# Kernel optimization log

Hardware: AMD Instinct MI355X
Metric: run time of the kernel (lower is better)

The kernel has to match this reference:

```python
import jax, jax.numpy as jnp
import numpy as np

K = 4

def grid_sample_bilinear_zeros(img, grid):
    # img: [b,c,H,W]; grid: [b,h,w,2] normalized coords (x,y) in [-1,1]
    # PyTorch grid_sample, mode='bilinear', padding_mode='zeros', align_corners=False
    b, c, H, W = img.shape
    h, w = grid.shape[1], grid.shape[2]
    ix = (grid[..., 0] + 1.0) * (W * 0.5) - 0.5
    iy = (grid[..., 1] + 1.0) * (H * 0.5) - 0.5
    x0 = jnp.floor(ix); y0 = jnp.floor(iy)
    wx1 = ix - x0; wx0 = 1.0 - wx1
    wy1 = iy - y0; wy0 = 1.0 - wy1
    x0i = x0.astype(jnp.int32); y0i = y0.astype(jnp.int32)
    x1i = x0i + 1; y1i = y0i + 1
    imgf = img.reshape(b, c, H * W)
    N = h * w

    def gather(xi, yi, wgt):
        valid = (xi >= 0) & (xi < W) & (yi >= 0) & (yi < H)
        xc = jnp.clip(xi, 0, W - 1); yc = jnp.clip(yi, 0, H - 1)
        idx = (yc * W + xc).reshape(b, 1, N)
        g = jnp.take_along_axis(imgf, jnp.broadcast_to(idx, (b, c, N)), axis=2)
        wv = (wgt * valid.astype(img.dtype)).reshape(b, 1, N)
        return g * wv

    out = (gather(x0i, y0i, wx0 * wy0) + gather(x1i, y0i, wx1 * wy0) +
           gather(x0i, y1i, wx0 * wy1) + gather(x1i, y1i, wx1 * wy1))
    return out.reshape(b, c, h, w)


def setup_inputs() -> dict:
    key = jax.random.key(0)
    ks = jax.random.split(key, 8)
    b, c, h, w = 8, 256, 96, 96
    out_ch = 256
    x = jax.random.normal(ks[0], (b, c, h, w), dtype=jnp.float32)
    Wc = jax.random.normal(ks[1], (out_ch, c), dtype=jnp.float32) * 0.02
    bc = jax.random.normal(ks[2], (out_ch,), dtype=jnp.float32) * 0.02
    Woff = jax.random.normal(ks[3], (K, 2, c), dtype=jnp.float32) * 0.02
    boff = jax.random.normal(ks[4], (K, 2), dtype=jnp.float32) * 0.02
    Wwt = jax.random.normal(ks[5], (K, c), dtype=jnp.float32) * 0.02
    bwt = jax.random.normal(ks[6], (K,), dtype=jnp.float32) * 0.02
    return {"x": x, "Wc": Wc, "bc": bc, "Woff": Woff, "boff": boff, "Wwt": Wwt, "bwt": bwt}


def reference(x, Wc, bc, Woff, boff, Wwt, bwt):
    b, c, h, w = x.shape
    # 1x1 conv projection
    proj = jnp.einsum('bchw,oc->bohw', x, Wc) + bc[None, :, None, None]
    # k flow fields, each [b,2,h,w] -> [k,b,h,w,2]
    flows = jnp.einsum('bchw,koc->kbohw', x, Woff) + boff[:, None, :, None, None]
    flows = jnp.transpose(flows, (0, 1, 3, 4, 2))
    # softmax sampling weights [b,k,h,w]
    logits = jnp.einsum('bchw,kc->bkhw', x, Wwt) + bwt[None, :, None, None]
    weights = jax.nn.softmax(logits, axis=1)
    # base pixel grid (x,y)
    gy, gx = jnp.meshgrid(jnp.arange(h, dtype=x.dtype), jnp.arange(w, dtype=x.dtype), indexing='ij')
    base = jnp.stack((gx, gy), axis=-1)  # [h,w,2]
    vgrid = base[None, None] + flows  # [k,b,h,w,2]
    vx = 2.0 * vgrid[..., 0] / max(w - 1, 1) - 1.0
    vy = 2.0 * vgrid[..., 1] / max(h - 1, 1) - 1.0
    vgrid_scaled = jnp.stack((vx, vy), axis=-1)  # [k,b,h,w,2]
    feats = jax.vmap(lambda g: grid_sample_bilinear_zeros(proj, g))(vgrid_scaled)  # [k,b,o,h,w]
    out = jnp.einsum('kbohw,bkhw->bohw', feats, weights)
    return out
```

## Files before the change

### kernel.cpp

```cpp
#include <hip/hip_runtime.h>

#define HW   9216
#define IMG  96
#define NB   8
#define NK   4

typedef __bf16 bf16x8 __attribute__((ext_vector_type(8)));
typedef float  f32x4  __attribute__((ext_vector_type(4)));

__device__ __forceinline__ unsigned short f2bf(float f) {
    unsigned int u = __float_as_uint(f);
    u += 0x7FFFu + ((u >> 16) & 1u);
    return (unsigned short)(u >> 16);
}

extern "C" __global__ __launch_bounds__(256, 4)
void prep_kernel(const float* __restrict__ x,
                 const float* __restrict__ Wc,
                 const float* __restrict__ Woff,
                 const float* __restrict__ boff,
                 const float* __restrict__ Wwt,
                 const float* __restrict__ bwt,
                 unsigned short* __restrict__ xbt,
                 unsigned short* __restrict__ Wcb,
                 float2* __restrict__ coords,
                 float* __restrict__ wts)
{
    __shared__ __align__(16) unsigned short tile[64 * 266];

    const int t   = threadIdx.x;
    const int bxr = blockIdx.x;

    if (bxr >= NB * 144) {
        int u = ((bxr - NB * 144) * 256 + t) * 4;
        float4 v = *(const float4*)(Wc + u);
        union { unsigned short h[4]; int2 p; } pk;
        pk.h[0] = f2bf(v.x); pk.h[1] = f2bf(v.y);
        pk.h[2] = f2bf(v.z); pk.h[3] = f2bf(v.w);
        *(int2*)(Wcb + u) = pk.p;
        return;
    }

    const int b  = bxr / 144;
    const int p0 = (bxr % 144) * 64;
    const int px = t & 63;
    const int g  = __builtin_amdgcn_readfirstlane(t >> 6);

    float acc[12];
    #pragma unroll
    for (int j = 0; j < 12; ++j) acc[j] = 0.f;

    const float* xb = x + ((size_t)(b * 256 + g * 64)) * HW + p0 + px;
    unsigned int* trow = (unsigned int*)tile;

    for (int i0 = 0; i0 < 64; i0 += 8) {
        float v[8];
        #pragma unroll
        for (int q = 0; q < 8; ++q)
            v[q] = xb[(size_t)(i0 + q) * HW];
        #pragma unroll
        for (int q = 0; q < 8; ++q) {
            const int c = g * 64 + i0 + q;
            #pragma unroll
            for (int j = 0; j < 8; ++j) acc[j] += v[q] * Woff[j * 256 + c];
            #pragma unroll
            for (int j = 0; j < 4; ++j) acc[8 + j] += v[q] * Wwt[j * 256 + c];
        }
        #pragma unroll
        for (int q = 0; q < 8; q += 2) {
            unsigned int pk = (unsigned int)f2bf(v[q]) | ((unsigned int)f2bf(v[q + 1]) << 16);
            trow[px * 133 + ((g * 64 + i0 + q) >> 1)] = pk;
        }
    }

    __syncthreads();
    #pragma unroll
    for (int r = 0; r < 8; ++r) {
        int u = t + 256 * r;
        int sub = u & 31, p2 = u >> 5;
        int4 v = *(const int4*)(tile + p2 * 266 + sub * 8);
        *(int4*)(xbt + ((size_t)b * HW + p0 + p2) * 256 + sub * 8) = v;
    }
    __syncthreads();

    float* red = (float*)tile;
    #pragma unroll
    for (int j = 0; j < 12; ++j)
        red[(g * 64 + px) * 12 + j] = acc[j];
    __syncthreads();

    if (t < 64) {
        float s[12];
        #pragma unroll
        for (int j = 0; j < 12; ++j)
            s[j] = red[(0 * 64 + px) * 12 + j] + red[(1 * 64 + px) * 12 + j] +
                   red[(2 * 64 + px) * 12 + j] + red[(3 * 64 + px) * 12 + j];

        const int p = p0 + px;
        const float pyf = (float)(p / IMG);
        const float pxf = (float)(p % IMG);

        #pragma unroll
        for (int k = 0; k < NK; ++k) {
            float fx = s[k * 2 + 0] + boff[k * 2 + 0];
            float fy = s[k * 2 + 1] + boff[k * 2 + 1];
            float vx = 2.0f * (pxf + fx) / 95.0f - 1.0f;
            float vy = 2.0f * (pyf + fy) / 95.0f - 1.0f;
            float ix = (vx + 1.0f) * 48.0f - 0.5f;
            float iy = (vy + 1.0f) * 48.0f - 0.5f;
            coords[((size_t)k * NB + b) * HW + p] = make_float2(ix, iy);
        }
        float l0 = s[8] + bwt[0], l1 = s[9] + bwt[1];
        float l2 = s[10] + bwt[2], l3 = s[11] + bwt[3];
        float m = fmaxf(fmaxf(l0, l1), fmaxf(l2, l3));
        float e0 = __expf(l0 - m), e1 = __expf(l1 - m);
        float e2 = __expf(l2 - m), e3 = __expf(l3 - m);
        float inv = 1.0f / (e0 + e1 + e2 + e3);
        wts[((size_t)0 * NB + b) * HW + p] = e0 * inv;
        wts[((size_t)1 * NB + b) * HW + p] = e1 * inv;
        wts[((size_t)2 * NB + b) * HW + p] = e2 * inv;
        wts[((size_t)3 * NB + b) * HW + p] = e3 * inv;
    }
}

extern "C" __global__ __launch_bounds__(256, 3)
void fused_kernel(const unsigned short* __restrict__ Wcb,
                  const unsigned short* __restrict__ xbt,
                  const float2* __restrict__ coords,
                  const float* __restrict__ wts,
                  const float* __restrict__ bc,
                  float* __restrict__ out)
{
    __shared__ __align__(16) unsigned char lds[49408];
    unsigned short* BsU   = (unsigned short*)lds;
    unsigned short* AsU   = (unsigned short*)(lds + 32768);
    float*          cw    = (float*)(lds + 32768);
    unsigned int*   ci    = (unsigned int*)(lds + 36864);
    float*          wsumL = (float*)(lds + 49152);

    const int t  = threadIdx.x;
    const int bx = blockIdx.x;
    const int b  = bx & 7;
    const int p0 = (bx >> 3) * 64;

    {
        const int px = t & 63;
        const int k  = t >> 6;
        const int p  = p0 + px;
        float2 cc = coords[((size_t)k * NB + b) * HW + p];
        float wk  = wts[((size_t)k * NB + b) * HW + p];
        float x0f = floorf(cc.x), y0f = floorf(cc.y);
        float wx1 = cc.x - x0f, wx0 = 1.0f - wx1;
        float wy1 = cc.y - y0f, wy0 = 1.0f - wy1;
        int x0 = (int)x0f, y0 = (int)y0f;
        int x1 = x0 + 1,   y1 = y0 + 1;
        float vx0 = (x0 >= 0 && x0 < IMG) ? 1.f : 0.f;
        float vx1 = (x1 >= 0 && x1 < IMG) ? 1.f : 0.f;
        float vy0 = (y0 >= 0 && y0 < IMG) ? 1.f : 0.f;
        float vy1 = (y1 >= 0 && y1 < IMG) ? 1.f : 0.f;
        int cx0 = min(max(x0, 0), IMG - 1), cx1 = min(max(x1, 0), IMG - 1);
        int cy0 = min(max(y0, 0), IMG - 1), cy1 = min(max(y1, 0), IMG - 1);
        int i0 = cy0 * IMG + cx0, i1 = cy0 * IMG + cx1;
        int i2 = cy1 * IMG + cx0, i3 = cy1 * IMG + cx1;
        float w0 = wk * wx0 * wy0 * vx0 * vy0;
        float w1 = wk * wx1 * wy0 * vx1 * vy0;
        float w2 = wk * wx0 * wy1 * vx0 * vy1;
        float w3 = wk * wx1 * wy1 * vx1 * vy1;
        *(float4*)(cw + px * 16 + k * 4) = make_float4(w0, w1, w2, w3);
        uint2 ip;
        ip.x = (unsigned int)i0 | ((unsigned int)i1 << 16);
        ip.y = (unsigned int)i2 | ((unsigned int)i3 << 16);
        *(uint2*)(ci + px * 8 + k * 2) = ip;
    }
    __syncthreads();

    {
        if (t < 64) {
            float s = 0.f;
            #pragma unroll
            for (int j = 0; j < 16; ++j) s += cw[t * 16 + j];
            wsumL[t] = s;
        }
        const int pxl = t >> 5, ch = t & 31;
        const unsigned short* gbase = xbt + (size_t)b * HW * 256 + ch * 8;
        #pragma unroll 2
        for (int rep = 0; rep < 8; ++rep) {
            const int px = rep * 8 + pxl;
            float wl[16];
            #pragma unroll
            for (int q = 0; q < 4; ++q) {
                float4 wv = *(const float4*)(cw + px * 16 + q * 4);
                wl[q * 4 + 0] = wv.x; wl[q * 4 + 1] = wv.y;
                wl[q * 4 + 2] = wv.z; wl[q * 4 + 3] = wv.w;
            }
            unsigned int ip[8];
            #pragma unroll
            for (int q = 0; q < 2; ++q) {
                uint4 iv = *(const uint4*)(ci + px * 8 + q * 4);
                ip[q * 4 + 0] = iv.x; ip[q * 4 + 1] = iv.y;
                ip[q * 4 + 2] = iv.z; ip[q * 4 + 3] = iv.w;
            }
            int4 v[16];
            #pragma unroll
            for (int j = 0; j < 16; ++j) {
                unsigned int idx = (ip[j >> 1] >> ((j & 1) * 16)) & 0xFFFFu;
                v[j] = *(const int4*)(gbase + (size_t)idx * 256);
            }
            float acc[8];
            #pragma unroll
            for (int i = 0; i < 8; ++i) acc[i] = 0.f;
            #pragma unroll
            for (int j = 0; j < 16; ++j) {
                const unsigned int* u = (const unsigned int*)&v[j];
                float wj = wl[j];
                #pragma unroll
                for (int q = 0; q < 4; ++q) {
                    float lo = __uint_as_float(u[q] << 16);
                    float hi = __uint_as_float(u[q] & 0xFFFF0000u);
                    acc[2 * q + 0] += wj * lo;
                    acc[2 * q + 1] += wj * hi;
                }
            }
            union { unsigned short h[8]; int4 v4; } pk;
            #pragma unroll
            for (int i = 0; i < 8; ++i) pk.h[i] = f2bf(acc[i]);
            const int pos = ch ^ (px & 7);
            *(int4*)(BsU + px * 256 + pos * 8) = pk.v4;
        }
    }
    __syncthreads();

    const int lane = t & 63, wave = t >> 6;
    const int wm = wave * 64;
    const int l15 = lane & 15, quad = lane >> 4;

    unsigned short* AsW = AsU + wave * 2048;

    f32x4 acc[4][4];
    #pragma unroll
    for (int mt = 0; mt < 4; ++mt)
        #pragma unroll
        for (int nt = 0; nt < 4; ++nt)
            acc[mt][nt] = (f32x4){0.f, 0.f, 0.f, 0.f};

#define STAGE_A(K0)                                                            \
    do {                                                                       \
        _Pragma("unroll")                                                      \
        for (int i_ = 0; i_ < 4; ++i_) {                                       \
            int u_ = lane + 64 * i_;                                           \
            int row_ = u_ >> 2, sub_ = u_ & 3;                                 \
            int subg_ = sub_ ^ ((row_ >> 1) & 3);                              \
            __builtin_amdgcn_global_load_lds(                                  \
                (const __attribute__((address_space(1))) void*)(               \
                    Wcb + (size_t)(wm + row_) * 256 + (K0) + subg_ * 8),       \
                (__attribute__((address_space(3))) void*)(AsW + u_ * 8),       \
                16, 0, 0);                                                     \
        }                                                                      \
    } while (0)

    STAGE_A(0);
    for (int k0 = 0; k0 < 256; k0 += 32) {
        asm volatile("s_waitcnt vmcnt(0)" ::: "memory");
        bf16x8 af[4], bf[4];
        #pragma unroll
        for (int mt = 0; mt < 4; ++mt) {
            int row = mt * 16 + l15;
            int pos = quad ^ ((row >> 1) & 3);
            af[mt] = *(const bf16x8*)(const void*)(AsW + row * 32 + pos * 8);
        }
        if (k0 + 32 < 256) {
            asm volatile("s_waitcnt lgkmcnt(0)" ::: "memory");
            __builtin_amdgcn_sched_barrier(0);
            STAGE_A(k0 + 32);
        }
        #pragma unroll
        for (int nt = 0; nt < 4; ++nt) {
            int row = nt * 16 + l15;
            int pos = ((k0 >> 3) + quad) ^ (row & 7);
            bf[nt] = *(const bf16x8*)(const void*)(BsU + row * 256 + pos * 8);
        }
        #pragma unroll
        for (int mt = 0; mt < 4; ++mt)
            #pragma unroll
            for (int nt = 0; nt < 4; ++nt)
                acc[mt][nt] = __builtin_amdgcn_mfma_f32_16x16x32_bf16(af[mt], bf[nt], acc[mt][nt], 0, 0, 0);
    }
#undef STAGE_A

    float wv[4];
    #pragma unroll
    for (int nt = 0; nt < 4; ++nt)
        wv[nt] = wsumL[nt * 16 + l15];

    #pragma unroll
    for (int mt = 0; mt < 4; ++mt) {
        int ob = wm + mt * 16 + quad * 4;
        #pragma unroll
        for (int reg = 0; reg < 4; ++reg) {
            int o = ob + reg;
            float bias = bc[o];
            float* dst = out + ((size_t)b * 256 + o) * HW + p0 + l15;
            #pragma unroll
            for (int nt = 0; nt < 4; ++nt)
                dst[nt * 16] = acc[mt][nt][reg] + bias * wv[nt];
        }
    }
}

extern "C" void kernel_launch(void* const* d_in, const int* in_sizes, int n_in,
                              void* d_out, int out_size, void* d_ws, size_t ws_size,
                              hipStream_t stream)
{
    const float* x    = (const float*)d_in[0];
    const float* Wc   = (const float*)d_in[1];
    const float* bc   = (const float*)d_in[2];
    const float* Woff = (const float*)d_in[3];
    const float* boff = (const float*)d_in[4];
    const float* Wwt  = (const float*)d_in[5];
    const float* bwt  = (const float*)d_in[6];
    float* out = (float*)d_out;

    char* ws = (char*)d_ws;
    unsigned short* xbt  = (unsigned short*)(ws);
    float2* coords       = (float2*)(ws + 37748736);
    float*  wts          = (float*)(ws + 40108032);
    unsigned short* Wcb  = (unsigned short*)(ws + 41287680);

    prep_kernel<<<dim3(NB * 144 + 64), dim3(256), 0, stream>>>(
        x, Wc, Woff, boff, Wwt, bwt, xbt, Wcb, coords, wts);
    fused_kernel<<<dim3(NB * 144), dim3(256), 0, stream>>>(
        Wcb, xbt, coords, wts, bc, out);
}
```

Before: 190.2 us.

## Double-buffer gather loads in fused kernel and widen prep blocks to 512 threads

```diff
diff --git a/kernel.cpp b/kernel.cpp
--- a/kernel.cpp
+++ b/kernel.cpp
@@ -14,7 +14,7 @@
     return (unsigned short)(u >> 16);
 }
 
-extern "C" __global__ __launch_bounds__(256, 4)
+extern "C" __global__ __launch_bounds__(512, 8)
 void prep_kernel(const float* __restrict__ x,
                  const float* __restrict__ Wc,
                  const float* __restrict__ Woff,
@@ -32,7 +32,7 @@
     const int bxr = blockIdx.x;
 
     if (bxr >= NB * 144) {
-        int u = ((bxr - NB * 144) * 256 + t) * 4;
+        int u = ((bxr - NB * 144) * 512 + t) * 4;
         float4 v = *(const float4*)(Wc + u);
         union { unsigned short h[4]; int2 p; } pk;
         pk.h[0] = f2bf(v.x); pk.h[1] = f2bf(v.y);
@@ -50,17 +50,17 @@
     #pragma unroll
     for (int j = 0; j < 12; ++j) acc[j] = 0.f;
 
-    const float* xb = x + ((size_t)(b * 256 + g * 64)) * HW + p0 + px;
+    const float* xb = x + ((size_t)(b * 256 + g * 32)) * HW + p0 + px;
     unsigned int* trow = (unsigned int*)tile;
 
-    for (int i0 = 0; i0 < 64; i0 += 8) {
+    for (int i0 = 0; i0 < 32; i0 += 8) {
         float v[8];
         #pragma unroll
         for (int q = 0; q < 8; ++q)
             v[q] = xb[(size_t)(i0 + q) * HW];
         #pragma unroll
         for (int q = 0; q < 8; ++q) {
-            const int c = g * 64 + i0 + q;
+            const int c = g * 32 + i0 + q;
             #pragma unroll
             for (int j = 0; j < 8; ++j) acc[j] += v[q] * Woff[j * 256 + c];
             #pragma unroll
@@ -69,14 +69,14 @@
         #pragma unroll
         for (int q = 0; q < 8; q += 2) {
             unsigned int pk = (unsigned int)f2bf(v[q]) | ((unsigned int)f2bf(v[q + 1]) << 16);
-            trow[px * 133 + ((g * 64 + i0 + q) >> 1)] = pk;
-        }
-    }
-
-    __syncthreads();
-    #pragma unroll
-    for (int r = 0; r < 8; ++r) {
-        int u = t + 256 * r;
+            trow[px * 133 + ((g * 32 + i0 + q) >> 1)] = pk;
+        }
+    }
+
+    __syncthreads();
+    #pragma unroll
+    for (int r = 0; r < 4; ++r) {
+        int u = t + 512 * r;
         int sub = u & 31, p2 = u >> 5;
         int4 v = *(const int4*)(tile + p2 * 266 + sub * 8);
         *(int4*)(xbt + ((size_t)b * HW + p0 + p2) * 256 + sub * 8) = v;
@@ -92,9 +92,13 @@
     if (t < 64) {
         float s[12];
         #pragma unroll
-        for (int j = 0; j < 12; ++j)
-            s[j] = red[(0 * 64 + px) * 12 + j] + red[(1 * 64 + px) * 12 + j] +
-                   red[(2 * 64 + px) * 12 + j] + red[(3 * 64 + px) * 12 + j];
+        for (int j = 0; j < 12; ++j) {
+            float sj = 0.f;
+            #pragma unroll
+            for (int w = 0; w < 8; ++w)
+                sj += red[(w * 64 + px) * 12 + j];
+            s[j] = sj;
+        }
 
         const int p = p0 + px;
         const float pyf = (float)(p / IMG);
@@ -183,50 +187,65 @@
         }
         const int pxl = t >> 5, ch = t & 31;
         const unsigned short* gbase = xbt + (size_t)b * HW * 256 + ch * 8;
-        #pragma unroll 2
+
+        int4  va[8], vb[8];
+        float wa[8], wb[8];
+
+#define ISSUE(BUF, WL, PX, GRP)                                               \
+        do {                                                                   \
+            uint4 iv_ = *(const uint4*)(ci + (PX) * 8 + (GRP) * 4);            \
+            unsigned id_[8] = { iv_.x & 0xFFFFu, iv_.x >> 16,                  \
+                                iv_.y & 0xFFFFu, iv_.y >> 16,                  \
+                                iv_.z & 0xFFFFu, iv_.z >> 16,                  \
+                                iv_.w & 0xFFFFu, iv_.w >> 16 };                \
+            _Pragma("unroll")                                                  \
+            for (int j_ = 0; j_ < 8; ++j_)                                     \
+                (BUF)[j_] = *(const int4*)(gbase + (size_t)id_[j_] * 256);     \
+            float4 w0_ = *(const float4*)(cw + (PX) * 16 + (GRP) * 8);         \
+            float4 w1_ = *(const float4*)(cw + (PX) * 16 + (GRP) * 8 + 4);     \
+            (WL)[0] = w0_.x; (WL)[1] = w0_.y; (WL)[2] = w0_.z; (WL)[3] = w0_.w;\
+            (WL)[4] = w1_.x; (WL)[5] = w1_.y; (WL)[6] = w1_.z; (WL)[7] = w1_.w;\
+        } while (0)
+
+#define CONSUME(BUF, WL, ACC)                                                  \
+        do {                                                                   \
+            _Pragma("unroll")                                                  \
+            for (int j_ = 0; j_ < 8; ++j_) {                                   \
+                const unsigned int* u_ = (const unsigned int*)&(BUF)[j_];      \
+                float wj_ = (WL)[j_];                                          \
+                _Pragma("unroll")                                              \
+                for (int q_ = 0; q_ < 4; ++q_) {                               \
+                    float lo_ = __uint_as_float(u_[q_] << 16);                 \
+                    float hi_ = __uint_as_float(u_[q_] & 0xFFFF0000u);         \
+                    (ACC)[2 * q_ + 0] += wj_ * lo_;                            \
+                    (ACC)[2 * q_ + 1] += wj_ * hi_;                            \
+                }                                                              \
+            }                                                                  \
+        } while (0)
+
+        ISSUE(va, wa, pxl, 0);
+        ISSUE(vb, wb, pxl, 1);
+
         for (int rep = 0; rep < 8; ++rep) {
-            const int px = rep * 8 + pxl;
-            float wl[16];
-            #pragma unroll
-            for (int q = 0; q < 4; ++q) {
-                float4 wv = *(const float4*)(cw + px * 16 + q * 4);
-                wl[q * 4 + 0] = wv.x; wl[q * 4 + 1] = wv.y;
-                wl[q * 4 + 2] = wv.z; wl[q * 4 + 3] = wv.w;
-            }
-            unsigned int ip[8];
-            #pragma unroll
-            for (int q = 0; q < 2; ++q) {
-                uint4 iv = *(const uint4*)(ci + px * 8 + q * 4);
-                ip[q * 4 + 0] = iv.x; ip[q * 4 + 1] = iv.y;
-                ip[q * 4 + 2] = iv.z; ip[q * 4 + 3] = iv.w;
-            }
-            int4 v[16];
-            #pragma unroll
-            for (int j = 0; j < 16; ++j) {
-                unsigned int idx = (ip[j >> 1] >> ((j & 1) * 16)) & 0xFFFFu;
-                v[j] = *(const int4*)(gbase + (size_t)idx * 256);
-            }
+            const int px  = rep * 8 + pxl;
+            const int pxn = px + 8;
             float acc[8];
             #pragma unroll
             for (int i = 0; i < 8; ++i) acc[i] = 0.f;
-            #pragma unroll
-            for (int j = 0; j < 16; ++j) {
-                const unsigned int* u = (const unsigned int*)&v[j];
-                float wj = wl[j];
-                #pragma unroll
-                for (int q = 0; q < 4; ++q) {
-                    float lo = __uint_as_float(u[q] << 16);
-                    float hi = __uint_as_float(u[q] & 0xFFFF0000u);
-                    acc[2 * q + 0] += wj * lo;
-                    acc[2 * q + 1] += wj * hi;
-                }
-            }
+
+            CONSUME(va, wa, acc);
+            if (rep < 7) ISSUE(va, wa, pxn, 0);
+            CONSUME(vb, wb, acc);
+            if (rep < 7) ISSUE(vb, wb, pxn, 1);
+
             union { unsigned short h[8]; int4 v4; } pk;
             #pragma unroll
             for (int i = 0; i < 8; ++i) pk.h[i] = f2bf(acc[i]);
             const int pos = ch ^ (px & 7);
             *(int4*)(BsU + px * 256 + pos * 8) = pk.v4;
         }
+#undef ISSUE
+#undef CONSUME
     }
     __syncthreads();
 
@@ -326,7 +345,7 @@
     float*  wts          = (float*)(ws + 40108032);
     unsigned short* Wcb  = (unsigned short*)(ws + 41287680);
 
-    prep_kernel<<<dim3(NB * 144 + 64), dim3(256), 0, stream>>>(
+    prep_kernel<<<dim3(NB * 144 + 32), dim3(512), 0, stream>>>(
         x, Wc, Woff, boff, Wwt, bwt, xbt, Wcb, coords, wts);
     fused_kernel<<<dim3(NB * 144), dim3(256), 0, stream>>>(
         Wcb, xbt, coords, wts, bc, out);
```

Result: slower. 230.5 us (+21.2%).
